# Optimization experiments

Hardware: AMD Instinct MI355X
Metric: run time of the kernel (lower is better)

The kernel has to match this reference:

```python
import jax, jax.numpy as jnp
import numpy as np

B, K, H, W = 16, 64, 28, 28
HID, OUT = 128, 128
FLAT = 64 * 4 * 4  # 28 -> (28-5)//2+1=12 -> (12-5)//2+1=4 after two 5x5 stride-2 VALID convs


def setup_inputs() -> dict:
    key = jax.random.key(0)
    ks = jax.random.split(key, 12)
    g = lambda k, shape, s=0.05: jax.random.normal(k, shape, dtype=jnp.float32) * s
    return {
        "x": jax.random.normal(ks[0], (B, K, H, W), dtype=jnp.float32),
        "conv1_w": g(ks[1], (32, 1, 5, 5)),
        "conv1_b": g(ks[2], (32,)),
        "conv2_w": g(ks[3], (64, 32, 5, 5)),
        "conv2_b": g(ks[4], (64,)),
        "fc_w": g(ks[5], (HID, FLAT)),
        "fc_b": g(ks[6], (HID,)),
        "coeffs": g(ks[7], (HID, OUT, 15), float(np.sqrt(2.0 / (HID + OUT)))),
        "eq_bias": g(ks[8], (OUT,)),
        "diag_bias": g(ks[9], (OUT,)),
        "out_w": g(ks[10], (1, OUT)),
        "out_b": g(ks[11], (1,)),
    }


def _conv(x, w, b, stride):
    y = jax.lax.conv_general_dilated(x, w, (stride, stride), 'VALID',
                                     dimension_numbers=('NCHW', 'OIHW', 'NCHW'))
    return y + b[None, :, None, None]


def _ops_2_to_2(P):
    # P: (B, D, m, m) -> (B, D, 15, m, m), Maron et al. basis, 'inf' normalization
    m = P.shape[-1]
    mf = jnp.asarray(m, P.dtype)
    I = jnp.eye(m, dtype=P.dtype)
    diag = jnp.diagonal(P, axis1=-2, axis2=-1)            # (B,D,m)
    sum_diag = diag.sum(-1, keepdims=True)                # (B,D,1)
    sum_rows = P.sum(-1)                                  # (B,D,m)
    sum_cols = P.sum(-2)                                  # (B,D,m)
    sum_all = P.sum((-2, -1))[..., None, None]            # (B,D,1,1)
    de = lambda v: v[..., None] * I                       # diag_embed
    bc = lambda v: jnp.broadcast_to(v, P.shape)
    op1 = de(diag)
    op2 = de(jnp.broadcast_to(sum_diag, diag.shape)) / mf
    op3 = de(sum_rows) / mf
    op4 = de(sum_cols) / mf
    op5 = de(jnp.broadcast_to(sum_all[..., 0], diag.shape)) / (mf * mf)
    op6 = bc(sum_cols[..., :, None]) / mf
    op7 = bc(sum_rows[..., :, None]) / mf
    op8 = bc(sum_cols[..., None, :]) / mf
    op9 = bc(sum_rows[..., None, :]) / mf
    op10 = P
    op11 = jnp.swapaxes(P, -1, -2)
    op12 = bc(diag[..., :, None])
    op13 = bc(diag[..., None, :])
    op14 = bc(sum_diag[..., None]) / mf
    op15 = bc(sum_all) / (mf * mf)
    return jnp.stack([op1, op2, op3, op4, op5, op6, op7, op8,
                      op9, op10, op11, op12, op13, op14, op15], axis=2)


def reference(x, conv1_w, conv1_b, conv2_w, conv2_b, fc_w, fc_b,
              coeffs, eq_bias, diag_bias, out_w, out_b):
    Bx, k, h, w = x.shape
    y = x.reshape(Bx * k, 1, h, w)
    y = jax.nn.relu(_conv(y, conv1_w, conv1_b, 2))
    y = jax.nn.relu(_conv(y, conv2_w, conv2_b, 2))
    y = y.reshape(Bx * k, -1) @ fc_w.T + fc_b              # (B*k, HID)
    feat = y.reshape(Bx, k, -1)                            # (B, k, D)
    P = jnp.einsum('bid,bjd->bdij', feat, feat)            # (B, D, k, k)
    ops = _ops_2_to_2(P)                                   # (B, D, 15, k, k)
    out = jnp.einsum('dsp,bdpij->bsij', coeffs, ops)       # (B, S, k, k)
    out = out + eq_bias[None, :, None, None]
    out = out + jnp.eye(k, dtype=out.dtype) * diag_bias[None, :, None, None]
    out = jax.nn.relu(out).mean((-2, -1))                  # (B, S)
    out = jax.nn.relu(out)                                 # dropout_prob=0 / eval: identity
    return out @ out_w.T + out_b                           # (B, 1)
```

## Files before the change

kernel.cpp:

```cpp
#include <hip/hip_runtime.h>


__global__ __launch_bounds__(256) void k_prep(
        const float* __restrict__ coeffs, const float* __restrict__ fc_w,
        const float* __restrict__ w2,
        float* __restrict__ CaT,  float* __restrict__ CdgT, float* __restrict__ CdrT,
        float* __restrict__ CugT, float* __restrict__ CurT,
        float* __restrict__ CvgT, float* __restrict__ CvrT,
        float* __restrict__ CctT, float* __restrict__ CcAT,
        float* __restrict__ CwtT, float* __restrict__ CwAT,
        float* __restrict__ fcwT, float* __restrict__ w2T,
        float* __restrict__ dout) {
    int idx = blockIdx.x * 256 + threadIdx.x;
    if (idx < 16384) {
        int d = idx >> 7, s = idx & 127;
        const float* c = coeffs + idx * 15;
        const float im = 1.0f / 64.0f, im2 = 1.0f / 4096.0f;
        int t = s * 128 + d;
        CaT[t]  = c[9] + c[10];
        CdgT[t] = c[0];
        CdrT[t] = (c[2] + c[3]) * im;
        CurT[t] = (c[5] + c[6]) * im;
        CugT[t] = c[11];
        CvrT[t] = (c[7] + c[8]) * im;
        CvgT[t] = c[12];
        CctT[t] = c[1] * im;
        CcAT[t] = c[4] * im2;
        CwtT[t] = c[13] * im;
        CwAT[t] = c[14] * im2;
        if (idx < 16) dout[idx] = 0.0f;
    } else if (idx < 16384 + 131072) {
        int e = idx - 16384;
        int s = e >> 10, k = e & 1023;
        fcwT[k * 128 + s] = fc_w[e];
    } else if (idx < 16384 + 131072 + 51200) {
        int e = idx - 147456;
        int oc = e & 63, r = e >> 6;
        w2T[e] = w2[oc * 800 + r];
    }
}

__global__ __launch_bounds__(256) void k_convfc(
        const float* __restrict__ x,  const float* __restrict__ w1,
        const float* __restrict__ b1, const float* __restrict__ w2T,
        const float* __restrict__ b2, const float* __restrict__ fcwT,
        const float* __restrict__ fc_b, float* __restrict__ feat) {
    __shared__ alignas(16) float xs[784];
    __shared__ float w1s[800];
    __shared__ alignas(16) float c1[32 * 144];
    __shared__ alignas(16) float ysh[1024];
    __shared__ float red[256];
    int n = blockIdx.x, tid = threadIdx.x;

    for (int i = tid; i < 784; i += 256) xs[i] = x[n * 784 + i];
    for (int i = tid; i < 800; i += 256) w1s[i] = w1[i];
    __syncthreads();

    for (int o = tid; o < 4608; o += 256) {
        int oc = o / 144, pos = o - oc * 144;
        int oy = pos / 12, ox = pos - oy * 12;
        const float* bp = xs + oy * 56 + ox * 2;
        const float* wp = w1s + oc * 25;
        float acc = b1[oc];
#pragma unroll
        for (int ky = 0; ky < 5; ++ky)
#pragma unroll
            for (int kx = 0; kx < 5; ++kx)
                acc = fmaf(bp[ky * 28 + kx], wp[ky * 5 + kx], acc);
        c1[o] = fmaxf(acc, 0.0f);
    }
    __syncthreads();

    {
        int oc = tid >> 2, q = tid & 3;
        float a0, a1, a2, a3;
        a0 = a1 = a2 = a3 = b2[oc];
        for (int ic = 0; ic < 32; ++ic) {
            const float* base = c1 + ic * 144 + q * 24;
            float wreg[25];
#pragma unroll
            for (int t = 0; t < 25; ++t) wreg[t] = w2T[(ic * 25 + t) * 64 + oc];
#pragma unroll
            for (int ky = 0; ky < 5; ++ky) {
                const float* rowp = base + ky * 12;
                float4 v0 = *(const float4*)(rowp);
                float4 v1 = *(const float4*)(rowp + 4);
                float4 v2 = *(const float4*)(rowp + 8);
                float r[12] = {v0.x, v0.y, v0.z, v0.w, v1.x, v1.y, v1.z, v1.w,
                               v2.x, v2.y, v2.z, v2.w};
#pragma unroll
                for (int kx = 0; kx < 5; ++kx) {
                    float wv = wreg[ky * 5 + kx];
                    a0 = fmaf(wv, r[kx],     a0);
                    a1 = fmaf(wv, r[2 + kx], a1);
                    a2 = fmaf(wv, r[4 + kx], a2);
                    a3 = fmaf(wv, r[6 + kx], a3);
                }
            }
        }
        int yb = oc * 16 + q * 4;
        ysh[yb]     = fmaxf(a0, 0.0f);
        ysh[yb + 1] = fmaxf(a1, 0.0f);
        ysh[yb + 2] = fmaxf(a2, 0.0f);
        ysh[yb + 3] = fmaxf(a3, 0.0f);
    }
    __syncthreads();

    {
        int s = tid & 127, h = tid >> 7;
        const float* bp2 = fcwT + (h * 512) * 128 + s;
        const float* yrow = ysh + h * 512;
        float acc = 0.0f;
#pragma unroll 8
        for (int k = 0; k < 512; ++k) acc = fmaf(yrow[k], bp2[k * 128], acc);
        red[tid] = acc;
        __syncthreads();
        if (h == 0) feat[n * 128 + s] = red[s] + red[s + 128] + fc_b[s];
    }
}

#define FS_IDX(r, d) (((r) << 7) + (((((d) >> 2) ^ (((r) >> 2) & 7))) << 2) + ((d) & 3))

__global__ __launch_bounds__(256) void k_main2(
        const float* __restrict__ feat,
        const float* __restrict__ CaT,  const float* __restrict__ CdgT,
        const float* __restrict__ CdrT, const float* __restrict__ CugT,
        const float* __restrict__ CurT, const float* __restrict__ CvgT,
        const float* __restrict__ CvrT, const float* __restrict__ CctT,
        const float* __restrict__ CcAT, const float* __restrict__ CwtT,
        const float* __restrict__ CwAT,
        const float* __restrict__ eq_bias, const float* __restrict__ diag_bias,
        const float* __restrict__ out_w,   const float* __restrict__ out_b,
        float* __restrict__ dout) {
    __shared__ alignas(16) float fs[8192];
    __shared__ alignas(16) float fa[8192];
    __shared__ float ash[128];
    __shared__ alignas(16) float Ssh[128];
    __shared__ float Uv[64], Vv[64], Dv[64];
    __shared__ float red[4];
    __shared__ float parts[4];
    int b = blockIdx.x >> 7, s = blockIdx.x & 127;
    int tid = threadIdx.x;
    const float* fb = feat + b * 8192;

    for (int i = tid; i < 8192; i += 256) {
        int r = i >> 7, d = i & 127;
        fs[FS_IDX(r, d)] = fb[i];
    }
    if (tid < 128) ash[tid] = CaT[s * 128 + tid];
    __syncthreads();

    for (int i = tid; i < 8192; i += 256) {
        int r = i >> 7, d = i & 127;
        int ii = FS_IDX(r, d);
        fa[ii] = fs[ii] * ash[d];
    }
    if (tid < 128) {
        int d = tid;
        float sv = 0.0f, tv = 0.0f;
        for (int r = 0; r < 64; ++r) {
            float v = fs[FS_IDX(r, d)];
            sv += v;
            tv = fmaf(v, v, tv);
        }
        Ssh[d] = sv;
        float av = sv * sv;
        float dcv = fmaf(CctT[s * 128 + d], tv, CcAT[s * 128 + d] * av);
        float wvv = fmaf(CwtT[s * 128 + d], tv, CwAT[s * 128 + d] * av);
#pragma unroll
        for (int m = 1; m < 64; m <<= 1) {
            dcv += __shfl_xor(dcv, m);
            wvv += __shfl_xor(wvv, m);
        }
        if ((tid & 63) == 0) {
            parts[tid >> 6] = dcv;
            parts[2 + (tid >> 6)] = wvv;
        }
    }
    __syncthreads();

    int tx = tid & 15, ty = tid >> 4;
    {
        int d0 = tx * 8;
        const float* cb = CdgT + s * 128 + d0;
        float4 cg0 = *(const float4*)(cb);
        float4 cg1 = *(const float4*)(cb + 4);
        cb = CdrT + s * 128 + d0;
        float4 cr0 = *(const float4*)(cb);
        float4 cr1 = *(const float4*)(cb + 4);
        cb = CugT + s * 128 + d0;
        float4 ug0 = *(const float4*)(cb);
        float4 ug1 = *(const float4*)(cb + 4);
        cb = CurT + s * 128 + d0;
        float4 ur0 = *(const float4*)(cb);
        float4 ur1 = *(const float4*)(cb + 4);
        cb = CvgT + s * 128 + d0;
        float4 vg0 = *(const float4*)(cb);
        float4 vg1 = *(const float4*)(cb + 4);
        cb = CvrT + s * 128 + d0;
        float4 vr0 = *(const float4*)(cb);
        float4 vr1 = *(const float4*)(cb + 4);
        float4 sv0 = *(const float4*)&Ssh[d0];
        float4 sv1 = *(const float4*)&Ssh[d0 + 4];
        float cg[8] = {cg0.x, cg0.y, cg0.z, cg0.w, cg1.x, cg1.y, cg1.z, cg1.w};
        float cr[8] = {cr0.x, cr0.y, cr0.z, cr0.w, cr1.x, cr1.y, cr1.z, cr1.w};
        float ug[8] = {ug0.x, ug0.y, ug0.z, ug0.w, ug1.x, ug1.y, ug1.z, ug1.w};
        float ur[8] = {ur0.x, ur0.y, ur0.z, ur0.w, ur1.x, ur1.y, ur1.z, ur1.w};
        float vg[8] = {vg0.x, vg0.y, vg0.z, vg0.w, vg1.x, vg1.y, vg1.z, vg1.w};
        float vr[8] = {vr0.x, vr0.y, vr0.z, vr0.w, vr1.x, vr1.y, vr1.z, vr1.w};
        float sv[8] = {sv0.x, sv0.y, sv0.z, sv0.w, sv1.x, sv1.y, sv1.z, sv1.w};
        float pD[4], pU[4], pV[4];
#pragma unroll
        for (int u = 0; u < 4; ++u) {
            int i = ty * 4 + u;
            float4 fA = *(const float4*)&fs[FS_IDX(i, d0)];
            float4 fB = *(const float4*)&fs[FS_IDX(i, d0 + 4)];
            float fv[8] = {fA.x, fA.y, fA.z, fA.w, fB.x, fB.y, fB.z, fB.w};
            float aD = 0.0f, aU = 0.0f, aV = 0.0f;
#pragma unroll
            for (int e = 0; e < 8; ++e) {
                float g  = fv[e] * fv[e];
                float rr = fv[e] * sv[e];
                aD = fmaf(cg[e], g, fmaf(cr[e], rr, aD));
                aU = fmaf(ug[e], g, fmaf(ur[e], rr, aU));
                aV = fmaf(vg[e], g, fmaf(vr[e], rr, aV));
            }
            pD[u] = aD; pU[u] = aU; pV[u] = aV;
        }
#pragma unroll
        for (int m = 1; m < 16; m <<= 1) {
#pragma unroll
            for (int u = 0; u < 4; ++u) {
                pD[u] += __shfl_xor(pD[u], m);
                pU[u] += __shfl_xor(pU[u], m);
                pV[u] += __shfl_xor(pV[u], m);
            }
        }
        if (tx == 0) {
#pragma unroll
            for (int u = 0; u < 4; ++u) {
                Dv[ty * 4 + u] = pD[u];
                Uv[ty * 4 + u] = pU[u];
                Vv[ty * 4 + u] = pV[u];
            }
        }
    }
    __syncthreads();

    float acc[4][4] = {};
#pragma unroll 2
    for (int d = 0; d < 128; d += 4) {
        float4 ai[4], bj[4];
#pragma unroll
        for (int u = 0; u < 4; ++u) ai[u] = *(const float4*)&fa[FS_IDX(ty * 4 + u, d)];
#pragma unroll
        for (int v = 0; v < 4; ++v) bj[v] = *(const float4*)&fs[FS_IDX(tx * 4 + v, d)];
#pragma unroll
        for (int u = 0; u < 4; ++u)
#pragma unroll
            for (int v = 0; v < 4; ++v)
                acc[u][v] += ai[u].x * bj[v].x + ai[u].y * bj[v].y +
                             ai[u].z * bj[v].z + ai[u].w * bj[v].w;
    }

    float sDc = parts[0] + parts[1] + diag_bias[s];
    float sW  = parts[2] + parts[3] + eq_bias[s];
    float psum = 0.0f;
#pragma unroll
    for (int u = 0; u < 4; ++u) {
        int i = ty * 4 + u;
#pragma unroll
        for (int v = 0; v < 4; ++v) {
            int j = tx * 4 + v;
            float val = acc[u][v] + Uv[i] + Vv[j] + sW;
            if (i == j) val += Dv[i] + sDc;
            psum += fmaxf(val, 0.0f);
        }
    }
#pragma unroll
    for (int m = 1; m < 64; m <<= 1) psum += __shfl_xor(psum, m);
    if ((tid & 63) == 0) red[tid >> 6] = psum;
    __syncthreads();
    if (tid == 0) {
        float tot = red[0] + red[1] + red[2] + red[3];
        float o1 = tot * (1.0f / 4096.0f);
        float o = fmaxf(o1, 0.0f) * out_w[s];
        if (s == 0) o += out_b[0];
        atomicAdd(dout + b, o);
    }
}

extern "C" void kernel_launch(void* const* d_in, const int* in_sizes, int n_in,
                              void* d_out, int out_size, void* d_ws, size_t ws_size,
                              hipStream_t stream) {
    const float* x      = (const float*)d_in[0];
    const float* w1     = (const float*)d_in[1];
    const float* b1     = (const float*)d_in[2];
    const float* w2     = (const float*)d_in[3];
    const float* b2     = (const float*)d_in[4];
    const float* fc_w   = (const float*)d_in[5];
    const float* fc_b   = (const float*)d_in[6];
    const float* coeffs = (const float*)d_in[7];
    const float* eqb    = (const float*)d_in[8];
    const float* dgb    = (const float*)d_in[9];
    const float* out_w  = (const float*)d_in[10];
    const float* out_b  = (const float*)d_in[11];

    float* ws = (float*)d_ws;
    float* feat = ws; ws += 131072;
    float* fcwT = ws; ws += 131072;
    float* w2T  = ws; ws += 51200;
    float* CaT  = ws; ws += 16384;
    float* CdgT = ws; ws += 16384;
    float* CdrT = ws; ws += 16384;
    float* CugT = ws; ws += 16384;
    float* CurT = ws; ws += 16384;
    float* CvgT = ws; ws += 16384;
    float* CvrT = ws; ws += 16384;
    float* CctT = ws; ws += 16384;
    float* CcAT = ws; ws += 16384;
    float* CwtT = ws; ws += 16384;
    float* CwAT = ws; ws += 16384;

    k_prep<<<776, 256, 0, stream>>>(coeffs, fc_w, w2,
                                    CaT, CdgT, CdrT, CugT, CurT, CvgT, CvrT,
                                    CctT, CcAT, CwtT, CwAT, fcwT, w2T,
                                    (float*)d_out);
    k_convfc<<<1024, 256, 0, stream>>>(x, w1, b1, w2T, b2, fcwT, fc_b, feat);
    k_main2<<<2048, 256, 0, stream>>>(feat, CaT, CdgT, CdrT, CugT, CurT,
                                      CvgT, CvrT, CctT, CcAT, CwtT, CwAT,
                                      eqb, dgb, out_w, out_b, (float*)d_out);
}
```

Measured before the change: 214.2 us.

## Batch two images per conv block and four output channels per main block

The conv/FC kernel now processes two images per block. It uses a register-tiled conv1 (one row of 12 outputs per thread), a channel-last conv2 layout with an input-channel split and shuffle reduction, and an FC stage that reuses each weight float4 across both images. The main kernel handles four output channels per block, so the feature tile load and row/column statistics are shared and the scaled copy is folded into the inner product. This is meant to cut redundant global weight reads and repeated feature loads, at the cost of more registers and fewer blocks (512 each) with launch bounds requesting 2 waves per SIMD.

```diff
diff --git a/kernel.cpp b/kernel.cpp
--- a/kernel.cpp
+++ b/kernel.cpp
@@ -1,5 +1,7 @@
 #include <hip/hip_runtime.h>
 
+
+#define FS_IDX(r, d) (((r) << 7) + (((((d) >> 2) ^ (((r) >> 2) & 7))) << 2) + ((d) & 3))
 
 __global__ __launch_bounds__(256) void k_prep(
         const float* __restrict__ coeffs, const float* __restrict__ fc_w,
@@ -9,7 +11,7 @@
         float* __restrict__ CvgT, float* __restrict__ CvrT,
         float* __restrict__ CctT, float* __restrict__ CcAT,
         float* __restrict__ CwtT, float* __restrict__ CwAT,
-        float* __restrict__ fcwT, float* __restrict__ w2T,
+        float* __restrict__ fcwT, float* __restrict__ w2R,
         float* __restrict__ dout) {
     int idx = blockIdx.x * 256 + threadIdx.x;
     if (idx < 16384) {
@@ -29,99 +31,170 @@
         CwtT[t] = c[13] * im;
         CwAT[t] = c[14] * im2;
         if (idx < 16) dout[idx] = 0.0f;
-    } else if (idx < 16384 + 131072) {
+    } else if (idx < 147456) {
         int e = idx - 16384;
         int s = e >> 10, k = e & 1023;
         fcwT[k * 128 + s] = fc_w[e];
-    } else if (idx < 16384 + 131072 + 51200) {
+    } else if (idx < 198656) {
         int e = idx - 147456;
-        int oc = e & 63, r = e >> 6;
-        w2T[e] = w2[oc * 800 + r];
+        int ic = e & 31;
+        int q = e >> 5;
+        int kx = q % 5, q2 = q / 5, ky = q2 % 5, oc = q2 / 5;
+        w2R[e] = w2[oc * 800 + ic * 25 + ky * 5 + kx];
     }
 }
 
-__global__ __launch_bounds__(256) void k_convfc(
+__global__ __launch_bounds__(256, 2) void k_convfc(
         const float* __restrict__ x,  const float* __restrict__ w1,
-        const float* __restrict__ b1, const float* __restrict__ w2T,
+        const float* __restrict__ b1, const float* __restrict__ w2R,
         const float* __restrict__ b2, const float* __restrict__ fcwT,
         const float* __restrict__ fc_b, float* __restrict__ feat) {
-    __shared__ alignas(16) float xs[784];
-    __shared__ float w1s[800];
-    __shared__ alignas(16) float c1[32 * 144];
-    __shared__ alignas(16) float ysh[1024];
-    __shared__ float red[256];
-    int n = blockIdx.x, tid = threadIdx.x;
-
-    for (int i = tid; i < 784; i += 256) xs[i] = x[n * 784 + i];
-    for (int i = tid; i < 800; i += 256) w1s[i] = w1[i];
-    __syncthreads();
-
-    for (int o = tid; o < 4608; o += 256) {
-        int oc = o / 144, pos = o - oc * 144;
-        int oy = pos / 12, ox = pos - oy * 12;
-        const float* bp = xs + oy * 56 + ox * 2;
-        const float* wp = w1s + oc * 25;
-        float acc = b1[oc];
-#pragma unroll
-        for (int ky = 0; ky < 5; ++ky)
-#pragma unroll
-            for (int kx = 0; kx < 5; ++kx)
-                acc = fmaf(bp[ky * 28 + kx], wp[ky * 5 + kx], acc);
-        c1[o] = fmaxf(acc, 0.0f);
-    }
-    __syncthreads();
+    __shared__ alignas(16) float xs[1568];
+    __shared__ alignas(16) float w1s[800];
+    __shared__ alignas(16) float c1T[4608];
+    __shared__ alignas(16) float ysh[2][1024];
+    __shared__ alignas(16) float ps[8][2][128];
+    int tid = threadIdx.x;
+    int n0 = blockIdx.x * 2;
 
     {
-        int oc = tid >> 2, q = tid & 3;
-        float a0, a1, a2, a3;
-        a0 = a1 = a2 = a3 = b2[oc];
-        for (int ic = 0; ic < 32; ++ic) {
-            const float* base = c1 + ic * 144 + q * 24;
-            float wreg[25];
-#pragma unroll
-            for (int t = 0; t < 25; ++t) wreg[t] = w2T[(ic * 25 + t) * 64 + oc];
+        const float4* xsrc = (const float4*)(x + n0 * 784);
+        float4* xdst = (float4*)xs;
+        for (int i = tid; i < 392; i += 256) xdst[i] = xsrc[i];
+        const float4* wsrc = (const float4*)w1;
+        float4* wdst = (float4*)w1s;
+        for (int i = tid; i < 200; i += 256) wdst[i] = wsrc[i];
+    }
+    __syncthreads();
+
+    for (int img = 0; img < 2; ++img) {
+        for (int task = tid; task < 384; task += 256) {
+            int oy = task >> 5, oc = task & 31;
+            const float* wp = w1s + oc * 25;
+            float wr[25];
+#pragma unroll
+            for (int t = 0; t < 25; ++t) wr[t] = wp[t];
+            float out[12];
+            float bv = b1[oc];
+#pragma unroll
+            for (int ox = 0; ox < 12; ++ox) out[ox] = bv;
+            const float* xb = xs + img * 784 + (oy * 2) * 28;
 #pragma unroll
             for (int ky = 0; ky < 5; ++ky) {
-                const float* rowp = base + ky * 12;
-                float4 v0 = *(const float4*)(rowp);
-                float4 v1 = *(const float4*)(rowp + 4);
-                float4 v2 = *(const float4*)(rowp + 8);
-                float r[12] = {v0.x, v0.y, v0.z, v0.w, v1.x, v1.y, v1.z, v1.w,
-                               v2.x, v2.y, v2.z, v2.w};
+                const float4* rp = (const float4*)(xb + ky * 28);
+                float4 r0 = rp[0], r1 = rp[1], r2 = rp[2], r3 = rp[3];
+                float4 r4 = rp[4], r5 = rp[5], r6 = rp[6];
+                float rf[28] = {r0.x, r0.y, r0.z, r0.w, r1.x, r1.y, r1.z, r1.w,
+                                r2.x, r2.y, r2.z, r2.w, r3.x, r3.y, r3.z, r3.w,
+                                r4.x, r4.y, r4.z, r4.w, r5.x, r5.y, r5.z, r5.w,
+                                r6.x, r6.y, r6.z, r6.w};
 #pragma unroll
                 for (int kx = 0; kx < 5; ++kx) {
-                    float wv = wreg[ky * 5 + kx];
-                    a0 = fmaf(wv, r[kx],     a0);
-                    a1 = fmaf(wv, r[2 + kx], a1);
-                    a2 = fmaf(wv, r[4 + kx], a2);
-                    a3 = fmaf(wv, r[6 + kx], a3);
-                }
-            }
-        }
-        int yb = oc * 16 + q * 4;
-        ysh[yb]     = fmaxf(a0, 0.0f);
-        ysh[yb + 1] = fmaxf(a1, 0.0f);
-        ysh[yb + 2] = fmaxf(a2, 0.0f);
-        ysh[yb + 3] = fmaxf(a3, 0.0f);
-    }
-    __syncthreads();
+                    float wv = wr[ky * 5 + kx];
+#pragma unroll
+                    for (int ox = 0; ox < 12; ++ox)
+                        out[ox] = fmaf(rf[2 * ox + kx], wv, out[ox]);
+                }
+            }
+#pragma unroll
+            for (int ox = 0; ox < 12; ++ox)
+                c1T[(oy * 12 + ox) * 32 + oc] = fmaxf(out[ox], 0.0f);
+        }
+        __syncthreads();
+
+        {
+            int icg = tid & 7, ocg = tid >> 3;
+            int ic0 = icg * 4;
+            float acc[2][16];
+#pragma unroll
+            for (int l = 0; l < 2; ++l)
+#pragma unroll
+                for (int p = 0; p < 16; ++p) acc[l][p] = 0.0f;
+#pragma unroll
+            for (int ky = 0; ky < 5; ++ky) {
+                float4 wv[2][5];
+#pragma unroll
+                for (int l = 0; l < 2; ++l) {
+                    int oc = ocg * 2 + l;
+#pragma unroll
+                    for (int kx = 0; kx < 5; ++kx)
+                        wv[l][kx] = *(const float4*)&w2R[((oc * 5 + ky) * 5 + kx) * 32 + ic0];
+                }
+#pragma unroll
+                for (int oyy = 0; oyy < 4; ++oyy) {
+                    int y = 2 * oyy + ky;
+                    float4 v[12];
+#pragma unroll
+                    for (int xx = 0; xx < 12; ++xx)
+                        v[xx] = *(const float4*)&c1T[(y * 12 + xx) * 32 + ic0];
+#pragma unroll
+                    for (int l = 0; l < 2; ++l)
+#pragma unroll
+                        for (int ox = 0; ox < 4; ++ox) {
+                            float s = acc[l][oyy * 4 + ox];
+#pragma unroll
+                            for (int kx = 0; kx < 5; ++kx) {
+                                float4 vv = v[2 * ox + kx];
+                                float4 ww = wv[l][kx];
+                                s = fmaf(vv.x, ww.x, s);
+                                s = fmaf(vv.y, ww.y, s);
+                                s = fmaf(vv.z, ww.z, s);
+                                s = fmaf(vv.w, ww.w, s);
+                            }
+                            acc[l][oyy * 4 + ox] = s;
+                        }
+                }
+            }
+#pragma unroll
+            for (int m = 1; m < 8; m <<= 1)
+#pragma unroll
+                for (int l = 0; l < 2; ++l)
+#pragma unroll
+                    for (int p = 0; p < 16; ++p)
+                        acc[l][p] += __shfl_xor(acc[l][p], m);
+            if (icg == 0) {
+#pragma unroll
+                for (int l = 0; l < 2; ++l) {
+                    int oc = ocg * 2 + l;
+                    float bb = b2[oc];
+#pragma unroll
+                    for (int p = 0; p < 16; ++p)
+                        ysh[img][oc * 16 + p] = fmaxf(acc[l][p] + bb, 0.0f);
+                }
+            }
+        }
+        __syncthreads();
+    }
 
     {
-        int s = tid & 127, h = tid >> 7;
-        const float* bp2 = fcwT + (h * 512) * 128 + s;
-        const float* yrow = ysh + h * 512;
-        float acc = 0.0f;
-#pragma unroll 8
-        for (int k = 0; k < 512; ++k) acc = fmaf(yrow[k], bp2[k * 128], acc);
-        red[tid] = acc;
-        __syncthreads();
-        if (h == 0) feat[n * 128 + s] = red[s] + red[s + 128] + fc_b[s];
+        int sg = tid & 31, kc = tid >> 5;
+        const float* yb0 = &ysh[0][kc * 128];
+        const float* yb1 = &ysh[1][kc * 128];
+        const float* wb = fcwT + kc * 128 * 128 + sg * 4;
+        float4 a0 = {0.f, 0.f, 0.f, 0.f}, a1 = {0.f, 0.f, 0.f, 0.f};
+#pragma unroll 4
+        for (int i = 0; i < 128; ++i) {
+            float4 w = *(const float4*)(wb + i * 128);
+            float y0 = yb0[i], y1 = yb1[i];
+            a0.x = fmaf(y0, w.x, a0.x); a0.y = fmaf(y0, w.y, a0.y);
+            a0.z = fmaf(y0, w.z, a0.z); a0.w = fmaf(y0, w.w, a0.w);
+            a1.x = fmaf(y1, w.x, a1.x); a1.y = fmaf(y1, w.y, a1.y);
+            a1.z = fmaf(y1, w.z, a1.z); a1.w = fmaf(y1, w.w, a1.w);
+        }
+        *(float4*)&ps[kc][0][sg * 4] = a0;
+        *(float4*)&ps[kc][1][sg * 4] = a1;
+    }
+    __syncthreads();
+    {
+        int img = tid >> 7, s = tid & 127;
+        float acc = fc_b[s];
+#pragma unroll
+        for (int kc = 0; kc < 8; ++kc) acc += ps[kc][img][s];
+        feat[(n0 + img) * 128 + s] = acc;
     }
 }
 
-#define FS_IDX(r, d) (((r) << 7) + (((((d) >> 2) ^ (((r) >> 2) & 7))) << 2) + ((d) & 3))
-
-__global__ __launch_bounds__(256) void k_main2(
+__global__ __launch_bounds__(256, 2) void k_main2(
         const float* __restrict__ feat,
         const float* __restrict__ CaT,  const float* __restrict__ CdgT,
         const float* __restrict__ CdrT, const float* __restrict__ CugT,
@@ -133,13 +206,13 @@
         const float* __restrict__ out_w,   const float* __restrict__ out_b,
         float* __restrict__ dout) {
     __shared__ alignas(16) float fs[8192];
-    __shared__ alignas(16) float fa[8192];
-    __shared__ float ash[128];
+    __shared__ alignas(16) float ash2[512];
     __shared__ alignas(16) float Ssh[128];
-    __shared__ float Uv[64], Vv[64], Dv[64];
-    __shared__ float red[4];
-    __shared__ float parts[4];
-    int b = blockIdx.x >> 7, s = blockIdx.x & 127;
+    __shared__ float Uv[4][64], Vv[4][64], Dv[4][64];
+    __shared__ float parts[2][8];
+    __shared__ float red[4][4];
+    int b = blockIdx.x >> 5, sq = blockIdx.x & 31;
+    int s0 = sq * 4;
     int tid = threadIdx.x;
     const float* fb = feat + b * 8192;
 
@@ -147,17 +220,15 @@
         int r = i >> 7, d = i & 127;
         fs[FS_IDX(r, d)] = fb[i];
     }
-    if (tid < 128) ash[tid] = CaT[s * 128 + tid];
-    __syncthreads();
-
-    for (int i = tid; i < 8192; i += 256) {
-        int r = i >> 7, d = i & 127;
-        int ii = FS_IDX(r, d);
-        fa[ii] = fs[ii] * ash[d];
-    }
+    for (int i = tid; i < 512; i += 256) {
+        int d = i >> 2, sl = i & 3;
+        ash2[d * 4 + sl] = CaT[(s0 + sl) * 128 + d];
+    }
+    __syncthreads();
+
     if (tid < 128) {
         int d = tid;
-        float sv = 0.0f, tv = 0.0f;
+        float sv = 0.f, tv = 0.f;
         for (int r = 0; r < 64; ++r) {
             float v = fs[FS_IDX(r, d)];
             sv += v;
@@ -165,16 +236,27 @@
         }
         Ssh[d] = sv;
         float av = sv * sv;
-        float dcv = fmaf(CctT[s * 128 + d], tv, CcAT[s * 128 + d] * av);
-        float wvv = fmaf(CwtT[s * 128 + d], tv, CwAT[s * 128 + d] * av);
-#pragma unroll
-        for (int m = 1; m < 64; m <<= 1) {
-            dcv += __shfl_xor(dcv, m);
-            wvv += __shfl_xor(wvv, m);
-        }
+        float dc[4], wv[4];
+#pragma unroll
+        for (int sl = 0; sl < 4; ++sl) {
+            int o = (s0 + sl) * 128 + d;
+            dc[sl] = fmaf(CctT[o], tv, CcAT[o] * av);
+            wv[sl] = fmaf(CwtT[o], tv, CwAT[o] * av);
+        }
+#pragma unroll
+        for (int m = 1; m < 64; m <<= 1)
+#pragma unroll
+            for (int sl = 0; sl < 4; ++sl) {
+                dc[sl] += __shfl_xor(dc[sl], m);
+                wv[sl] += __shfl_xor(wv[sl], m);
+            }
         if ((tid & 63) == 0) {
-            parts[tid >> 6] = dcv;
-            parts[2 + (tid >> 6)] = wvv;
+            int w = tid >> 6;
+#pragma unroll
+            for (int sl = 0; sl < 4; ++sl) {
+                parts[w][sl] = dc[sl];
+                parts[w][4 + sl] = wv[sl];
+            }
         }
     }
     __syncthreads();
@@ -182,110 +264,128 @@
     int tx = tid & 15, ty = tid >> 4;
     {
         int d0 = tx * 8;
-        const float* cb = CdgT + s * 128 + d0;
-        float4 cg0 = *(const float4*)(cb);
-        float4 cg1 = *(const float4*)(cb + 4);
-        cb = CdrT + s * 128 + d0;
-        float4 cr0 = *(const float4*)(cb);
-        float4 cr1 = *(const float4*)(cb + 4);
-        cb = CugT + s * 128 + d0;
-        float4 ug0 = *(const float4*)(cb);
-        float4 ug1 = *(const float4*)(cb + 4);
-        cb = CurT + s * 128 + d0;
-        float4 ur0 = *(const float4*)(cb);
-        float4 ur1 = *(const float4*)(cb + 4);
-        cb = CvgT + s * 128 + d0;
-        float4 vg0 = *(const float4*)(cb);
-        float4 vg1 = *(const float4*)(cb + 4);
-        cb = CvrT + s * 128 + d0;
-        float4 vr0 = *(const float4*)(cb);
-        float4 vr1 = *(const float4*)(cb + 4);
-        float4 sv0 = *(const float4*)&Ssh[d0];
-        float4 sv1 = *(const float4*)&Ssh[d0 + 4];
-        float cg[8] = {cg0.x, cg0.y, cg0.z, cg0.w, cg1.x, cg1.y, cg1.z, cg1.w};
-        float cr[8] = {cr0.x, cr0.y, cr0.z, cr0.w, cr1.x, cr1.y, cr1.z, cr1.w};
-        float ug[8] = {ug0.x, ug0.y, ug0.z, ug0.w, ug1.x, ug1.y, ug1.z, ug1.w};
-        float ur[8] = {ur0.x, ur0.y, ur0.z, ur0.w, ur1.x, ur1.y, ur1.z, ur1.w};
-        float vg[8] = {vg0.x, vg0.y, vg0.z, vg0.w, vg1.x, vg1.y, vg1.z, vg1.w};
-        float vr[8] = {vr0.x, vr0.y, vr0.z, vr0.w, vr1.x, vr1.y, vr1.z, vr1.w};
-        float sv[8] = {sv0.x, sv0.y, sv0.z, sv0.w, sv1.x, sv1.y, sv1.z, sv1.w};
-        float pD[4], pU[4], pV[4];
+        float4 s0v = *(const float4*)&Ssh[d0];
+        float4 s1v = *(const float4*)&Ssh[d0 + 4];
+        float sv[8] = {s0v.x, s0v.y, s0v.z, s0v.w, s1v.x, s1v.y, s1v.z, s1v.w};
+#pragma unroll
+        for (int sl = 0; sl < 4; ++sl) {
+            int o = (s0 + sl) * 128 + d0;
+            float4 A0, A1;
+#define LD8(arr, p) A0 = *(const float4*)&arr[o]; A1 = *(const float4*)&arr[o + 4]; \
+            float p[8] = {A0.x, A0.y, A0.z, A0.w, A1.x, A1.y, A1.z, A1.w};
+            LD8(CdgT, cg) LD8(CdrT, cr) LD8(CugT, ug) LD8(CurT, ur) LD8(CvgT, vg) LD8(CvrT, vr)
+#undef LD8
+            float pD[4], pU[4], pV[4];
+#pragma unroll
+            for (int u = 0; u < 4; ++u) {
+                int i = ty * 4 + u;
+                float4 fA = *(const float4*)&fs[FS_IDX(i, d0)];
+                float4 fB = *(const float4*)&fs[FS_IDX(i, d0 + 4)];
+                float fv[8] = {fA.x, fA.y, fA.z, fA.w, fB.x, fB.y, fB.z, fB.w};
+                float aD = 0.f, aU = 0.f, aV = 0.f;
+#pragma unroll
+                for (int e = 0; e < 8; ++e) {
+                    float g = fv[e] * fv[e];
+                    float rr = fv[e] * sv[e];
+                    aD = fmaf(cg[e], g, fmaf(cr[e], rr, aD));
+                    aU = fmaf(ug[e], g, fmaf(ur[e], rr, aU));
+                    aV = fmaf(vg[e], g, fmaf(vr[e], rr, aV));
+                }
+                pD[u] = aD; pU[u] = aU; pV[u] = aV;
+            }
+#pragma unroll
+            for (int m = 1; m < 16; m <<= 1)
+#pragma unroll
+                for (int u = 0; u < 4; ++u) {
+                    pD[u] += __shfl_xor(pD[u], m);
+                    pU[u] += __shfl_xor(pU[u], m);
+                    pV[u] += __shfl_xor(pV[u], m);
+                }
+            if (tx == 0)
+#pragma unroll
+                for (int u = 0; u < 4; ++u) {
+                    Dv[sl][ty * 4 + u] = pD[u];
+                    Uv[sl][ty * 4 + u] = pU[u];
+                    Vv[sl][ty * 4 + u] = pV[u];
+                }
+        }
+    }
+    __syncthreads();
+
+    float acc[4][16];
+#pragma unroll
+    for (int sl = 0; sl < 4; ++sl)
+#pragma unroll
+        for (int q = 0; q < 16; ++q) acc[sl][q] = 0.f;
+    for (int d = 0; d < 128; d += 4) {
+        float aif[4][4], bjf[4][4], a4f[4][4];
 #pragma unroll
         for (int u = 0; u < 4; ++u) {
-            int i = ty * 4 + u;
-            float4 fA = *(const float4*)&fs[FS_IDX(i, d0)];
-            float4 fB = *(const float4*)&fs[FS_IDX(i, d0 + 4)];
-            float fv[8] = {fA.x, fA.y, fA.z, fA.w, fB.x, fB.y, fB.z, fB.w};
-            float aD = 0.0f, aU = 0.0f, aV = 0.0f;
-#pragma unroll
-            for (int e = 0; e < 8; ++e) {
-                float g  = fv[e] * fv[e];
-                float rr = fv[e] * sv[e];
-                aD = fmaf(cg[e], g, fmaf(cr[e], rr, aD));
-                aU = fmaf(ug[e], g, fmaf(ur[e], rr, aU));
-                aV = fmaf(vg[e], g, fmaf(vr[e], rr, aV));
-            }
-            pD[u] = aD; pU[u] = aU; pV[u] = aV;
-        }
-#pragma unroll
-        for (int m = 1; m < 16; m <<= 1) {
-#pragma unroll
-            for (int u = 0; u < 4; ++u) {
-                pD[u] += __shfl_xor(pD[u], m);
-                pU[u] += __shfl_xor(pU[u], m);
-                pV[u] += __shfl_xor(pV[u], m);
-            }
-        }
-        if (tx == 0) {
-#pragma unroll
-            for (int u = 0; u < 4; ++u) {
-                Dv[ty * 4 + u] = pD[u];
-                Uv[ty * 4 + u] = pU[u];
-                Vv[ty * 4 + u] = pV[u];
-            }
-        }
-    }
-    __syncthreads();
-
-    float acc[4][4] = {};
-#pragma unroll 2
-    for (int d = 0; d < 128; d += 4) {
-        float4 ai[4], bj[4];
-#pragma unroll
-        for (int u = 0; u < 4; ++u) ai[u] = *(const float4*)&fa[FS_IDX(ty * 4 + u, d)];
-#pragma unroll
-        for (int v = 0; v < 4; ++v) bj[v] = *(const float4*)&fs[FS_IDX(tx * 4 + v, d)];
-#pragma unroll
-        for (int u = 0; u < 4; ++u)
-#pragma unroll
-            for (int v = 0; v < 4; ++v)
-                acc[u][v] += ai[u].x * bj[v].x + ai[u].y * bj[v].y +
-                             ai[u].z * bj[v].z + ai[u].w * bj[v].w;
-    }
-
-    float sDc = parts[0] + parts[1] + diag_bias[s];
-    float sW  = parts[2] + parts[3] + eq_bias[s];
-    float psum = 0.0f;
+            float4 t = *(const float4*)&fs[FS_IDX(ty * 4 + u, d)];
+            aif[u][0] = t.x; aif[u][1] = t.y; aif[u][2] = t.z; aif[u][3] = t.w;
+        }
+#pragma unroll
+        for (int v = 0; v < 4; ++v) {
+            float4 t = *(const float4*)&fs[FS_IDX(tx * 4 + v, d)];
+            bjf[v][0] = t.x; bjf[v][1] = t.y; bjf[v][2] = t.z; bjf[v][3] = t.w;
+        }
+#pragma unroll
+        for (int dd = 0; dd < 4; ++dd) {
+            float4 t = *(const float4*)&ash2[(d + dd) * 4];
+            a4f[dd][0] = t.x; a4f[dd][1] = t.y; a4f[dd][2] = t.z; a4f[dd][3] = t.w;
+        }
+#pragma unroll
+        for (int dd = 0; dd < 4; ++dd)
+#pragma unroll
+            for (int sl = 0; sl < 4; ++sl)
+#pragma unroll
+                for (int u = 0; u < 4; ++u) {
+                    float t = aif[u][dd] * a4f[dd][sl];
+#pragma unroll
+                    for (int v = 0; v < 4; ++v)
+                        acc[sl][u * 4 + v] = fmaf(t, bjf[v][dd], acc[sl][u * 4 + v]);
+                }
+    }
+
+    float sDc[4], sW[4];
+#pragma unroll
+    for (int sl = 0; sl < 4; ++sl) {
+        sDc[sl] = parts[0][sl] + parts[1][sl] + diag_bias[s0 + sl];
+        sW[sl]  = parts[0][4 + sl] + parts[1][4 + sl] + eq_bias[s0 + sl];
+    }
+    float psum[4] = {0.f, 0.f, 0.f, 0.f};
 #pragma unroll
     for (int u = 0; u < 4; ++u) {
         int i = ty * 4 + u;
 #pragma unroll
         for (int v = 0; v < 4; ++v) {
             int j = tx * 4 + v;
-            float val = acc[u][v] + Uv[i] + Vv[j] + sW;
-            if (i == j) val += Dv[i] + sDc;
-            psum += fmaxf(val, 0.0f);
-        }
-    }
-#pragma unroll
-    for (int m = 1; m < 64; m <<= 1) psum += __shfl_xor(psum, m);
-    if ((tid & 63) == 0) red[tid >> 6] = psum;
+#pragma unroll
+            for (int sl = 0; sl < 4; ++sl) {
+                float val = acc[sl][u * 4 + v] + Uv[sl][i] + Vv[sl][j] + sW[sl];
+                if (i == j) val += Dv[sl][i] + sDc[sl];
+                psum[sl] += fmaxf(val, 0.0f);
+            }
+        }
+    }
+#pragma unroll
+    for (int m = 1; m < 64; m <<= 1)
+#pragma unroll
+        for (int sl = 0; sl < 4; ++sl) psum[sl] += __shfl_xor(psum[sl], m);
+    if ((tid & 63) == 0) {
+        int w = tid >> 6;
+#pragma unroll
+        for (int sl = 0; sl < 4; ++sl) red[w][sl] = psum[sl];
+    }
     __syncthreads();
     if (tid == 0) {
-        float tot = red[0] + red[1] + red[2] + red[3];
-        float o1 = tot * (1.0f / 4096.0f);
-        float o = fmaxf(o1, 0.0f) * out_w[s];
-        if (s == 0) o += out_b[0];
+        float o = 0.f;
+#pragma unroll
+        for (int sl = 0; sl < 4; ++sl) {
+            float tot = red[0][sl] + red[1][sl] + red[2][sl] + red[3][sl];
+            o += fmaxf(tot * (1.0f / 4096.0f), 0.0f) * out_w[s0 + sl];
+        }
+        if (s0 == 0) o += out_b[0];
         atomicAdd(dout + b, o);
     }
 }
@@ -309,7 +409,7 @@
     float* ws = (float*)d_ws;
     float* feat = ws; ws += 131072;
     float* fcwT = ws; ws += 131072;
-    float* w2T  = ws; ws += 51200;
+    float* w2R  = ws; ws += 51200;
     float* CaT  = ws; ws += 16384;
     float* CdgT = ws; ws += 16384;
     float* CdrT = ws; ws += 16384;
@@ -324,10 +424,10 @@
 
     k_prep<<<776, 256, 0, stream>>>(coeffs, fc_w, w2,
                                     CaT, CdgT, CdrT, CugT, CurT, CvgT, CvrT,
-                                    CctT, CcAT, CwtT, CwAT, fcwT, w2T,
+                                    CctT, CcAT, CwtT, CwAT, fcwT, w2R,
                                     (float*)d_out);
-    k_convfc<<<1024, 256, 0, stream>>>(x, w1, b1, w2T, b2, fcwT, fc_b, feat);
-    k_main2<<<2048, 256, 0, stream>>>(feat, CaT, CdgT, CdrT, CugT, CurT,
-                                      CvgT, CvrT, CctT, CcAT, CwtT, CwAT,
-                                      eqb, dgb, out_w, out_b, (float*)d_out);
+    k_convfc<<<512, 256, 0, stream>>>(x, w1, b1, w2R, b2, fcwT, fc_b, feat);
+    k_main2<<<512, 256, 0, stream>>>(feat, CaT, CdgT, CdrT, CugT, CurT,
+                                     CvgT, CvrT, CctT, CcAT, CwtT, CwAT,
+                                     eqb, dgb, out_w, out_b, (float*)d_out);
 }
```

New measurement: 206.5 us. -3.6%, faster.
